# Performance work log

Hardware: AMD Instinct MI355X
Metric: run time of the kernel (lower is better)

The kernel has to match this reference:

```python
import math
import jax, jax.numpy as jnp
import numpy as np

C_CURV = 0.5  # Poincare ball curvature c (StablePoincareBall default)


def expmap0(u, c=C_CURV):
    """StablePoincareBall.expmap0: tangent at origin -> ball, with norm clamps."""
    sqrt_c = math.sqrt(c)
    u_norm = jnp.clip(jnp.linalg.norm(u, axis=-1, keepdims=True), 1e-8, 5.0)
    res = jnp.tanh(sqrt_c * u_norm) / sqrt_c * (u / u_norm)
    max_allowed = 0.95 / sqrt_c
    rn = jnp.linalg.norm(res, axis=-1, keepdims=True)
    scale = jnp.where(rn > max_allowed, max_allowed / rn, jnp.ones_like(rn))
    return res * scale


def poincare_pairwise_dist(x, p, c=C_CURV):
    """Geodesic dist d(x_i, p_j) = (2/sqrt(c)) atanh(sqrt(c) ||(-x) (+) p||).
    Uses the closed form for ||mobius_add(-x, p)||^2 in terms of ||x||^2, ||p||^2,
    <x,p> so only [B,C] intermediates are formed (no [B,C,D] broadcast).
    """
    x2 = jnp.sum(x * x, axis=-1, keepdims=True)        # [B,1]
    p2 = jnp.sum(p * p, axis=-1)[None, :]              # [1,C]
    mdot = -(x @ p.T)                                  # <-x, p>  [B,C]
    A = 1.0 + 2.0 * c * mdot + c * p2                  # coeff of (-x)
    Bc = 1.0 - c * x2                                  # coeff of p
    den = 1.0 + 2.0 * c * mdot + (c * c) * x2 * p2
    num2 = A * A * x2 + 2.0 * A * Bc * mdot + Bc * Bc * p2
    m2 = jnp.maximum(num2, 0.0) / jnp.maximum(den * den, 1e-15)
    sqrt_c = math.sqrt(c)
    arg = jnp.clip(sqrt_c * jnp.sqrt(m2 + 1e-15), 0.0, 1.0 - 1e-5)
    return (2.0 / sqrt_c) * jnp.arctanh(arg)


def setup_inputs() -> dict:
    key = jax.random.key(0)
    k1, k2 = jax.random.split(key)
    B, C, D = 128, 4096, 1024
    # inputs live on the Poincare ball: map random tangents via expmap0
    x = expmap0(0.5 * jax.random.normal(k1, (B, D), dtype=jnp.float32))
    # prototypes per __init__: expmap0(randn*0.1) then rescale norm to 1/sqrt(c)-1e-5
    init_tangent = 0.1 * jax.random.normal(k2, (C, D), dtype=jnp.float32)
    protos = expmap0(init_tangent)
    max_norm = 1.0 / math.sqrt(C_CURV) - 1e-5
    nrm = jnp.clip(jnp.linalg.norm(protos, axis=-1, keepdims=True), 1e-8)
    protos = protos * (max_norm / nrm)
    return {"x": x, "prototypes": protos}


def reference(x, prototypes):
    # logits = -geodesic distance to each class prototype, [B, num_classes]
    return -poincare_pairwise_dist(x, prototypes)
```

## Files before the change

### kernel.cpp

```cpp
#include <hip/hip_runtime.h>
#include <hip/hip_bf16.h>
#include <math.h>


#define DDIM 1024
#define CDIM 4096
#define BDIM 128

using f32x4  = __attribute__((ext_vector_type(4))) float;
using bf16x8 = __attribute__((ext_vector_type(8))) short;

__device__ inline ushort toBfU(float f) {
  __hip_bfloat16 h = __float2bfloat16(f);
  return *reinterpret_cast<ushort*>(&h);
}

__global__ __launch_bounds__(512) void x_frag(
    const float* __restrict__ x, ushort* __restrict__ xb, float* __restrict__ x2) {
  __shared__ __align__(16) char lds[16 * 2048];
  __shared__ float wpart[8][8];

  const int tid  = threadIdx.x;
  const int lane = tid & 63;
  const int w    = tid >> 6;
  const int qp   = blockIdx.x;
  const float* xp = x + (size_t)qp * 16 * DDIM;

  const int h    = tid >> 8;
  const int kcol = (tid & 255) * 4;

  float sq[8];
  #pragma unroll
  for (int it = 0; it < 8; ++it) {
    const int row = it * 2 + h;
    const f32x4 v = *(const f32x4*)(xp + (size_t)row * DDIM + kcol);
    float a = v[0] * v[0];
    a = fmaf(v[1], v[1], a); a = fmaf(v[2], v[2], a); a = fmaf(v[3], v[3], a);
    sq[it] = a;
    ushort4 o = { toBfU(v[0]), toBfU(v[1]), toBfU(v[2]), toBfU(v[3]) };
    const int kb = kcol * 2;
    *(ushort4*)&lds[row * 2048 + (kb ^ ((row & 7) << 4))] = o;
  }
  #pragma unroll
  for (int it = 0; it < 8; ++it) {
    float a = sq[it];
    #pragma unroll
    for (int off = 32; off > 0; off >>= 1) a += __shfl_xor(a, off, 64);
    if (lane == 0) wpart[w][it] = a;
  }
  __syncthreads();
  if (tid < 16) {
    const int hh = tid & 1, it = tid >> 1, wb = hh * 4;
    x2[qp * 16 + tid] =
        wpart[wb][it] + wpart[wb + 1][it] + wpart[wb + 2][it] + wpart[wb + 3][it];
  }
  #pragma unroll
  for (int i = 0; i < 4; ++i) {
    const int widx = tid + i * 512;
    const int t = widx >> 6, l = widx & 63, row = l & 15;
    const int kb16 = t * 64 + (l >> 4) * 16;
    const bf16x8 v = *(const bf16x8*)&lds[row * 2048 + (kb16 ^ ((row & 7) << 4))];
    *(bf16x8*)((char*)xb + ((size_t)qp * 2048 + widx) * 16) = v;
  }
}

__global__ __launch_bounds__(256) void hyper_frag(
    const ushort* __restrict__ xb, const float* __restrict__ p,
    const float* __restrict__ x2a, float* __restrict__ out) {
  __shared__ __align__(16) char ps[2][4096];
  __shared__ float p2s[16];
  __shared__ float x2l[64];

  const int tid  = threadIdx.x;
  const int lane = tid & 63;
  const int w    = __builtin_amdgcn_readfirstlane(tid >> 6);
  const int r15  = lane & 15, g = lane >> 4;

  const int bid = blockIdx.x;
  const int swz = ((bid & 7) << 6) | (bid >> 3);
  const int cg = swz >> 1, rg = swz & 1;
  const int rbase = rg * 64, cbase = cg * 16;

  const char* ga = (const char*)xb + ((size_t)(rg * 4 + w) * 2048 + lane) * 16;

  const int col = tid >> 4, o = tid & 15;
  const float* gp = p + (size_t)(cbase + col) * DDIM + o * 8;
  const int pw = col * 256 + ((o ^ (col & 7)) << 4);

  f32x4 acc = {0.f, 0.f, 0.f, 0.f};
  float p2p = 0.f;
  f32x4 pa0, pa1;
  bf16x8 aA[2][4];

#define ISSUE_A(c, ph)                                                         \
  { _Pragma("unroll")                                                          \
    for (int s = 0; s < 4; ++s)                                                \
      aA[ph][s] = *(const bf16x8*)(ga + ((c) * 4 + s) * 1024); }

#define ISSUE_P(c)                                                             \
  { pa0 = *(const f32x4*)(gp + (c) * 128);                                     \
    pa1 = *(const f32x4*)(gp + (c) * 128 + 4); }

#define WRITE_P(buf)                                                           \
  { p2p = fmaf(pa0[0], pa0[0], p2p); p2p = fmaf(pa0[1], pa0[1], p2p);          \
    p2p = fmaf(pa0[2], pa0[2], p2p); p2p = fmaf(pa0[3], pa0[3], p2p);          \
    p2p = fmaf(pa1[0], pa1[0], p2p); p2p = fmaf(pa1[1], pa1[1], p2p);          \
    p2p = fmaf(pa1[2], pa1[2], p2p); p2p = fmaf(pa1[3], pa1[3], p2p);          \
    bf16x8 _t;                                                                 \
    _t[0] = (short)toBfU(pa0[0]); _t[1] = (short)toBfU(pa0[1]);                \
    _t[2] = (short)toBfU(pa0[2]); _t[3] = (short)toBfU(pa0[3]);                \
    _t[4] = (short)toBfU(pa1[0]); _t[5] = (short)toBfU(pa1[1]);                \
    _t[6] = (short)toBfU(pa1[2]); _t[7] = (short)toBfU(pa1[3]);                \
    *(bf16x8*)&ps[buf][pw] = _t; }

#define COMPUTE(buf, ph)                                                       \
  { _Pragma("unroll")                                                          \
    for (int s = 0; s < 4; ++s) {                                              \
      const int off = ((s * 4 + g) ^ (r15 & 7)) << 4;                          \
      const bf16x8 b = *(const bf16x8*)&ps[buf][r15 * 256 + off];              \
      acc = __builtin_amdgcn_mfma_f32_16x16x32_bf16(aA[ph][s], b, acc, 0, 0, 0); \
    } }

  if (tid < 64) x2l[tid] = x2a[rbase + tid];
  ISSUE_A(0, 0)
  ISSUE_P(0)
  WRITE_P(0)

  #pragma unroll
  for (int c = 0; c < 8; ++c) {
    __syncthreads();
    if (c < 7) { ISSUE_A(c + 1, (c + 1) & 1) ISSUE_P(c + 1) }
    COMPUTE(c & 1, c & 1)
    if (c < 7) WRITE_P((c + 1) & 1)
  }

  p2p += __shfl_xor(p2p, 8, 64);
  p2p += __shfl_xor(p2p, 4, 64);
  p2p += __shfl_xor(p2p, 2, 64);
  p2p += __shfl_xor(p2p, 1, 64);
  if ((lane & 15) == 0) p2s[col] = p2p;
  __syncthreads();

  const float p2 = p2s[r15];
  #pragma unroll
  for (int i = 0; i < 4; ++i) {
    const int  rloc = (w << 4) + (g << 2) + i;
    const float dot = acc[i];
    const float x2  = x2l[rloc];
    const float A   = 1.0f - dot + 0.5f  * p2;
    const float Bc  = 1.0f - 0.5f * x2;
    const float den = 1.0f - dot + 0.25f * x2 * p2;
    float num2 = A * A * x2 - 2.0f * A * Bc * dot + Bc * Bc * p2;
    float m2   = fmaxf(num2, 0.0f) / fmaxf(den * den, 1e-15f);
    float arg  = fminf(0.7071067811865476f * sqrtf(m2 + 1e-15f), 0.99999f);
    out[(size_t)(rbase + rloc) * CDIM + cbase + r15] =
        -1.4142135623730951f * __logf((1.0f + arg) / (1.0f - arg));
  }
}

extern "C" void kernel_launch(void* const* d_in, const int* in_sizes, int n_in,
                              void* d_out, int out_size, void* d_ws, size_t ws_size,
                              hipStream_t stream) {
  const float* x = (const float*)d_in[0];
  const float* p = (const float*)d_in[1];
  float* out = (float*)d_out;

  ushort* xb = (ushort*)d_ws;
  float*  x2 = (float*)((char*)d_ws + (size_t)8 * 2048 * 16);

  x_frag<<<dim3(8), dim3(512), 0, stream>>>(x, xb, x2);
  hyper_frag<<<dim3(512), dim3(256), 0, stream>>>(xb, p, x2, out);
}
```

Before: 16.13 us.

## Fuse x preprocessing into main kernel using global atomic counter barrier

Removes the separate x_frag launch. The first 128 blocks of the main kernel each convert one row of x to bf16 fragments and compute its squared norm, then signal a global atomic counter. All blocks prefetch their prototype tile and spin until the counter reaches 128 before loading x fragments. This removes one kernel launch and its boundary, but adds a memset, a grid-wide spin-wait that relies on all 512 blocks being co-resident, and adds the x conversion work to 128 of the blocks.

```diff
diff --git a/kernel.cpp b/kernel.cpp
--- a/kernel.cpp
+++ b/kernel.cpp
@@ -15,58 +15,12 @@
   return *reinterpret_cast<ushort*>(&h);
 }
 
-__global__ __launch_bounds__(512) void x_frag(
-    const float* __restrict__ x, ushort* __restrict__ xb, float* __restrict__ x2) {
-  __shared__ __align__(16) char lds[16 * 2048];
-  __shared__ float wpart[8][8];
-
-  const int tid  = threadIdx.x;
-  const int lane = tid & 63;
-  const int w    = tid >> 6;
-  const int qp   = blockIdx.x;
-  const float* xp = x + (size_t)qp * 16 * DDIM;
-
-  const int h    = tid >> 8;
-  const int kcol = (tid & 255) * 4;
-
-  float sq[8];
-  #pragma unroll
-  for (int it = 0; it < 8; ++it) {
-    const int row = it * 2 + h;
-    const f32x4 v = *(const f32x4*)(xp + (size_t)row * DDIM + kcol);
-    float a = v[0] * v[0];
-    a = fmaf(v[1], v[1], a); a = fmaf(v[2], v[2], a); a = fmaf(v[3], v[3], a);
-    sq[it] = a;
-    ushort4 o = { toBfU(v[0]), toBfU(v[1]), toBfU(v[2]), toBfU(v[3]) };
-    const int kb = kcol * 2;
-    *(ushort4*)&lds[row * 2048 + (kb ^ ((row & 7) << 4))] = o;
-  }
-  #pragma unroll
-  for (int it = 0; it < 8; ++it) {
-    float a = sq[it];
-    #pragma unroll
-    for (int off = 32; off > 0; off >>= 1) a += __shfl_xor(a, off, 64);
-    if (lane == 0) wpart[w][it] = a;
-  }
-  __syncthreads();
-  if (tid < 16) {
-    const int hh = tid & 1, it = tid >> 1, wb = hh * 4;
-    x2[qp * 16 + tid] =
-        wpart[wb][it] + wpart[wb + 1][it] + wpart[wb + 2][it] + wpart[wb + 3][it];
-  }
-  #pragma unroll
-  for (int i = 0; i < 4; ++i) {
-    const int widx = tid + i * 512;
-    const int t = widx >> 6, l = widx & 63, row = l & 15;
-    const int kb16 = t * 64 + (l >> 4) * 16;
-    const bf16x8 v = *(const bf16x8*)&lds[row * 2048 + (kb16 ^ ((row & 7) << 4))];
-    *(bf16x8*)((char*)xb + ((size_t)qp * 2048 + widx) * 16) = v;
-  }
-}
-
-__global__ __launch_bounds__(256) void hyper_frag(
-    const ushort* __restrict__ xb, const float* __restrict__ p,
-    const float* __restrict__ x2a, float* __restrict__ out) {
+__global__ __launch_bounds__(256, 2) void hyper_sync(
+    const float* __restrict__ x, const float* __restrict__ p,
+    ushort* __restrict__ xb, float* __restrict__ x2g,
+    unsigned* __restrict__ cnt, float* __restrict__ out) {
+  __shared__ __align__(16) ushort xrow[1024];
+  __shared__ float rpart[4];
   __shared__ __align__(16) char ps[2][4096];
   __shared__ float p2s[16];
   __shared__ float x2l[64];
@@ -75,17 +29,16 @@
   const int lane = tid & 63;
   const int w    = __builtin_amdgcn_readfirstlane(tid >> 6);
   const int r15  = lane & 15, g = lane >> 4;
+  const int bid  = blockIdx.x;
 
-  const int bid = blockIdx.x;
   const int swz = ((bid & 7) << 6) | (bid >> 3);
   const int cg = swz >> 1, rg = swz & 1;
   const int rbase = rg * 64, cbase = cg * 16;
 
-  const char* ga = (const char*)xb + ((size_t)(rg * 4 + w) * 2048 + lane) * 16;
-
   const int col = tid >> 4, o = tid & 15;
   const float* gp = p + (size_t)(cbase + col) * DDIM + o * 8;
   const int pw = col * 256 + ((o ^ (col & 7)) << 4);
+  const char* ga = (const char*)xb + ((size_t)(rg * 4 + w) * 2048 + lane) * 16;
 
   f32x4 acc = {0.f, 0.f, 0.f, 0.f};
   float p2p = 0.f;
@@ -121,10 +74,41 @@
       acc = __builtin_amdgcn_mfma_f32_16x16x32_bf16(aA[ph][s], b, acc, 0, 0, 0); \
     } }
 
-  if (tid < 64) x2l[tid] = x2a[rbase + tid];
+  ISSUE_P(0)
+
+  if (bid < BDIM) {
+    const int r = bid;
+    const f32x4 v = *(const f32x4*)(x + (size_t)r * DDIM + tid * 4);
+    float a = v[0] * v[0];
+    a = fmaf(v[1], v[1], a); a = fmaf(v[2], v[2], a); a = fmaf(v[3], v[3], a);
+    ushort4 ov = { toBfU(v[0]), toBfU(v[1]), toBfU(v[2]), toBfU(v[3]) };
+    *(ushort4*)&xrow[tid * 4] = ov;
+    #pragma unroll
+    for (int off = 32; off > 0; off >>= 1) a += __shfl_xor(a, off, 64);
+    if (lane == 0) rpart[w] = a;
+    __syncthreads();
+    if (tid < 128) {
+      const bf16x8 wv = *(const bf16x8*)&xrow[tid * 8];
+      const size_t word = (size_t)(r >> 4) * 2048 + (tid >> 2) * 64 + (tid & 3) * 16 + (r & 15);
+      *(bf16x8*)((char*)xb + word * 16) = wv;
+    }
+    if (tid == 0) x2g[r] = rpart[0] + rpart[1] + rpart[2] + rpart[3];
+    __threadfence();
+    __syncthreads();
+    if (tid == 0)
+      __hip_atomic_fetch_add(cnt, 1u, __ATOMIC_RELEASE, __HIP_MEMORY_SCOPE_AGENT);
+  }
+
+  WRITE_P(0)
+
+  if (tid == 0) {
+    while (__hip_atomic_load(cnt, __ATOMIC_ACQUIRE, __HIP_MEMORY_SCOPE_AGENT) < 128u)
+      __builtin_amdgcn_s_sleep(8);
+  }
+  __syncthreads();
+
+  if (tid < 64) x2l[tid] = x2g[rbase + tid];
   ISSUE_A(0, 0)
-  ISSUE_P(0)
-  WRITE_P(0)
 
   #pragma unroll
   for (int c = 0; c < 8; ++c) {
@@ -165,9 +149,10 @@
   const float* p = (const float*)d_in[1];
   float* out = (float*)d_out;
 
-  ushort* xb = (ushort*)d_ws;
-  float*  x2 = (float*)((char*)d_ws + (size_t)8 * 2048 * 16);
+  ushort*   xb  = (ushort*)d_ws;
+  float*    x2  = (float*)((char*)d_ws + 262144);
+  unsigned* cnt = (unsigned*)((char*)d_ws + 262656);
 
-  x_frag<<<dim3(8), dim3(512), 0, stream>>>(x, xb, x2);
-  hyper_frag<<<dim3(512), dim3(256), 0, stream>>>(xb, p, x2, out);
+  hipMemsetAsync(cnt, 0, 4, stream);
+  hyper_sync<<<dim3(512), dim3(256), 0, stream>>>(x, p, xb, x2, cnt, out);
 }
```

Measured after the change: 52.74 us. 3.27x slower.
